# Kernel tuning notes

Measured on AMD Instinct MI355X. Metric: run time of the kernel, lower is better.

Reference implementation:

```python
import jax, jax.numpy as jnp
import numpy as np

B, HP, WP, EMB = 32, 56, 56, 256
HEADS, WX, WY = 8, 7, 7
WS = WX * WY

# relative position index table (constant int lookup, matches torch buffer)
_idx = np.indices((WX, WY)).transpose(1, 2, 0).reshape(WS, 2)
_REL = _idx[None, :, :] - _idx[:, None, :] + np.array([WX - 1, WY - 1])  # [49,49,2]

# shift masks (constants)
_m = WX * (WY // 2)
_row = np.zeros((WS, WS), np.float32)
_row[-_m:, :-_m] = -np.inf
_row[:-_m, -_m:] = -np.inf
# rearrange '(r w1) (c w2) -> (w1 r) (w2 c)' with w1=WX, w2=WY
_col = _row.reshape(WS // WX, WX, WS // WY, WY).transpose(1, 0, 3, 2).reshape(WS, WS)
ROW_MASK = jnp.asarray(_row)
COL_MASK = jnp.asarray(_col)


def setup_inputs() -> dict:
    key = jax.random.key(0)
    k1, k2, k3 = jax.random.split(key, 3)
    x = jax.random.normal(k1, (B, HP, WP, EMB), jnp.float32)
    w1 = jax.random.normal(k2, (EMB, 3 * EMB), jnp.float32) * 0.02
    b1 = jnp.zeros((3 * EMB,), jnp.float32)
    pos_emb = jax.random.normal(k3, (2 * WX - 1, 2 * WY - 1), jnp.float32)
    return {"x": x, "w1": w1, "b1": b1, "pos_emb": pos_emb}


def reference(x, w1, b1, pos_emb):
    Bn, H, W, E = x.shape
    e = E // HEADS
    hdim = float(E) / HEADS
    qkv = x @ w1 + b1                         # [B,H,W,3E]
    qkv = qkv.reshape(Bn, H, W, E, 3)         # (c k): c outer, k inner (interleaved QKV)
    # shifted: roll by (-WX)//2 = -4 for WX=7 (Python floor div, as in source)
    qkv = jnp.roll(qkv, ((-WX) // 2, (-WY) // 2), axis=(1, 2))
    Wh, Ww = H // WX, W // WY
    # split channel (e H): head index is INNER dim, as in source rearrange
    t = qkv.reshape(Bn, Wh, WX, Ww, WY, e, HEADS, 3)
    t = t.transpose(0, 6, 1, 3, 2, 4, 5, 7).reshape(Bn, HEADS, Wh, Ww, WS, e, 3)
    q, k, v = t[..., 0], t[..., 1], t[..., 2]
    attn = jnp.einsum('bhuvqe,bhuvke->bhuvqk', q, k) / jnp.sqrt(
        jnp.asarray(hdim, x.dtype))
    bias = pos_emb[_REL[:, :, 0], _REL[:, :, 1]]   # [49,49]
    attn = attn + bias
    # shift masks on last window row / last window column (corner gets both)
    attn = attn.at[:, :, -1, :, :, :].add(ROW_MASK)
    attn = attn.at[:, :, :, -1, :, :].add(COL_MASK)
    out = jnp.einsum('bhuvqk,bhuvke->bhuvqe', jax.nn.softmax(attn, axis=-1), v)
    # merge back: channel = e*HEADS + h
    out = out.reshape(Bn, HEADS, Wh, Ww, WX, WY, e)
    out = out.transpose(0, 2, 4, 3, 5, 6, 1).reshape(Bn, H, W, E)
    # reverse roll uses WX//2 = +3 (NOT the inverse of -4), faithful to source
    out = jnp.roll(out, (WX // 2, WY // 2), axis=(1, 2))
    return out
```

## Files before the change

### kernel.cpp

```cpp
#include <hip/hip_runtime.h>


typedef short bf16x8 __attribute__((ext_vector_type(8)));
typedef float f32x4 __attribute__((ext_vector_type(4)));
typedef unsigned short u16;
typedef u16 u16x8 __attribute__((ext_vector_type(8)));

#define MFMA16(A, B, C) __builtin_amdgcn_mfma_f32_16x16x32_bf16((A), (B), (C), 0, 0, 0)

__device__ __forceinline__ u16 f2bf(float f) {
  union { float f; unsigned int u; } c; c.f = f;
  unsigned int uu = c.u;
  return (u16)((uu + 0x7fffu + ((uu >> 16) & 1u)) >> 16);
}

#define OFF_A   32768
#define OFF_POS 65536
#define SMEM_BYTES (65536 + 704)

__global__ void prep_w(const float* __restrict__ w1, const float* __restrict__ b1,
                       u16* __restrict__ wT, float* __restrict__ bp) {
  int g = blockIdx.x * 256 + threadIdx.x;
  float val = w1[g];
  int n = g % 768;
  int k = g / 768;
  int t = n % 3, c = n / 3;
  int np = (c & 7) * 96 + t * 32 + (c >> 3);
  wT[np * 256 + k] = f2bf(val);
  if (g < 768) {
    int t2 = g % 3, c2 = g / 3;
    bp[(c2 & 7) * 96 + t2 * 32 + (c2 >> 3)] = b1[g];
  }
}

__launch_bounds__(512, 4)
__global__ void swin_fused(const float* __restrict__ x, const u16* __restrict__ wT,
                           const float* __restrict__ bp, const float* __restrict__ pos,
                           float* __restrict__ out) {
  __shared__ __align__(16) char smem[SMEM_BYTES];
  const int tid  = threadIdx.x;
  const int wave = tid >> 6;
  const int lane = tid & 63;
  const int quad = lane >> 4;
  const int l16  = lane & 15;
  const int blk  = blockIdx.x;
  const int b = blk >> 6, u = (blk >> 3) & 7, v = blk & 7;

  float* sPos = (float*)(smem + OFF_POS);
  if (tid < 169) sPos[tid] = pos[tid];

  {
    const int xbase = b * (56 * 56 * 256);
#pragma unroll
    for (int it = 0; it < 4; ++it) {
      int idx = tid + it * 512;
      int row = idx >> 5;
      int ck  = idx & 31;
      char* dst = smem + OFF_A + row * 512 + ((ck ^ (row & 7)) << 4);
      u16x8 val{};
      if (row < 49) {
        int i = row / 7, j = row % 7;
        int sh = u * 7 + i + 4; if (sh >= 56) sh -= 56;
        int sw = v * 7 + j + 4; if (sw >= 56) sw -= 56;
        const float4* src = (const float4*)(x + xbase + (sh * 56 + sw) * 256 + ck * 8);
        float4 f0 = src[0];
        float4 f1 = src[1];
        val.s0 = f2bf(f0.x); val.s1 = f2bf(f0.y); val.s2 = f2bf(f0.z); val.s3 = f2bf(f0.w);
        val.s4 = f2bf(f1.x); val.s5 = f2bf(f1.y); val.s6 = f2bf(f1.z); val.s7 = f2bf(f1.w);
      }
      *(u16x8*)dst = val;
    }
  }

  float bias[6];
#pragma unroll
  for (int i = 0; i < 6; ++i) bias[i] = bp[wave * 96 + i * 16 + l16];

  __syncthreads();

  const char* sA = smem + OFF_A;
  char* T = smem + wave * 4096;
  bf16x8 qf[4], kf[4], vf[2][2];

#pragma unroll
  for (int t = 0; t < 3; ++t) {
    f32x4 acc[4][2];
#pragma unroll
    for (int m = 0; m < 4; ++m) {
      acc[m][0] = (f32x4){0.f, 0.f, 0.f, 0.f};
      acc[m][1] = (f32x4){0.f, 0.f, 0.f, 0.f};
    }
    const u16* gB0 = wT + (wave * 96 + t * 32 + l16) * 256 + quad * 8;
    const u16* gB1 = gB0 + 16 * 256;
    bf16x8 b0 = *(const bf16x8*)gB0;
    bf16x8 b1 = *(const bf16x8*)gB1;
#pragma unroll
    for (int ks = 0; ks < 8; ++ks) {
      bf16x8 a[4];
#pragma unroll
      for (int m = 0; m < 4; ++m) {
        int row = m * 16 + l16;
        a[m] = *(const bf16x8*)(sA + row * 512 + (((ks * 4 + quad) ^ (row & 7)) << 4));
      }
      bf16x8 b0n, b1n;
      if (ks < 7) {
        b0n = *(const bf16x8*)(gB0 + (ks + 1) * 32);
        b1n = *(const bf16x8*)(gB1 + (ks + 1) * 32);
      }
#pragma unroll
      for (int m = 0; m < 4; ++m) {
        acc[m][0] = MFMA16(a[m], b0, acc[m][0]);
        acc[m][1] = MFMA16(a[m], b1, acc[m][1]);
      }
      if (ks < 7) { b0 = b0n; b1 = b1n; }
    }

    if (t < 2) {
#pragma unroll
      for (int m = 0; m < 4; ++m)
#pragma unroll
        for (int r = 0; r < 4; ++r) {
          int row = m * 16 + quad * 4 + r;
          int sw = (row >> 2) & 3;
          char* base = T + row * 64;
          *(u16*)(base + ((((l16 >> 3) ^ sw) << 4) | ((l16 & 7) << 1)))
              = f2bf(acc[m][0][r] + bias[t * 2]);
          *(u16*)(base + (((((l16 >> 3) + 2) ^ sw) << 4) | ((l16 & 7) << 1)))
              = f2bf(acc[m][1][r] + bias[t * 2 + 1]);
        }
      asm volatile("s_waitcnt lgkmcnt(0)" ::: "memory");
#pragma unroll
      for (int m = 0; m < 4; ++m) {
        int row = m * 16 + l16;
        const bf16x8 fr = *(const bf16x8*)(T + row * 64 + ((quad ^ ((row >> 2) & 3)) << 4));
        if (t == 0) qf[m] = fr; else kf[m] = fr;
      }
      asm volatile("s_waitcnt lgkmcnt(0)" ::: "memory");
    } else {
#pragma unroll
      for (int m = 0; m < 4; ++m)
#pragma unroll
        for (int r = 0; r < 4; ++r) {
          int key = m * 16 + quad * 4 + r;
          int kc = key >> 3, kb = (key & 7) << 1;
#pragma unroll
          for (int i = 0; i < 2; ++i) {
            int ch = i * 16 + l16;
            *(u16*)(T + ch * 128 + (((kc ^ (ch & 7)) << 4) | kb))
                = f2bf(acc[m][i][r] + bias[4 + i]);
          }
        }
      asm volatile("s_waitcnt lgkmcnt(0)" ::: "memory");
    }
  }

#pragma unroll
  for (int ph = 0; ph < 2; ++ph)
#pragma unroll
    for (int n = 0; n < 2; ++n) {
      int ch = n * 16 + l16;
      vf[ph][n] = *(const bf16x8*)(T + ch * 128 + (((ph * 4 + quad) ^ (ch & 7)) << 4));
    }
  asm volatile("s_waitcnt lgkmcnt(0)" ::: "memory");

  int ki[4], kj[4]; bool kok[4], kro[4], kco[4];
#pragma unroll
  for (int n = 0; n < 4; ++n) {
    int k = n * 16 + l16;
    ki[n] = k / 7; kj[n] = k % 7;
    kok[n] = (k < 49);
    kro[n] = (ki[n] >= 4);
    kco[n] = (kj[n] >= 4);
  }
  const bool rowm = (u == 7), colm = (v == 7);
  const float scale = 0.17677669529663687f;

  f32x4 o[4][2];
  {
    char* T2 = T;
#pragma unroll
    for (int m = 0; m < 4; ++m) {
      f32x4 s[4];
#pragma unroll
      for (int n = 0; n < 4; ++n)
        s[n] = MFMA16(qf[m], kf[n], ((f32x4){0.f, 0.f, 0.f, 0.f}));

      float inv[4];
#pragma unroll
      for (int r = 0; r < 4; ++r) {
        int q = m * 16 + quad * 4 + r;
        int qi = q / 7, qj = q % 7;
        bool qro = (qi >= 4), qco = (qj >= 4);
        float vmax = -3e30f;
#pragma unroll
        for (int n = 0; n < 4; ++n) {
          bool bad = (!kok[n]) || (rowm && (qro != kro[n])) || (colm && (qco != kco[n]));
          float sv = bad ? -1e30f
                         : s[n][r] * scale + sPos[(ki[n] - qi + 6) * 13 + (kj[n] - qj + 6)];
          s[n][r] = sv;
          vmax = fmaxf(vmax, sv);
        }
        vmax = fmaxf(vmax, __shfl_xor(vmax, 1));
        vmax = fmaxf(vmax, __shfl_xor(vmax, 2));
        vmax = fmaxf(vmax, __shfl_xor(vmax, 4));
        vmax = fmaxf(vmax, __shfl_xor(vmax, 8));
        float sum = 0.f;
#pragma unroll
        for (int n = 0; n < 4; ++n) {
          float p = __expf(s[n][r] - vmax);
          s[n][r] = p;
          sum += p;
        }
        sum += __shfl_xor(sum, 1);
        sum += __shfl_xor(sum, 2);
        sum += __shfl_xor(sum, 4);
        sum += __shfl_xor(sum, 8);
        inv[r] = 1.f / sum;
      }

#pragma unroll
      for (int n = 0; n < 4; ++n)
#pragma unroll
        for (int r = 0; r < 4; ++r) {
          int row16 = quad * 4 + r;
          int ch = (2 * n + (l16 >> 3) + row16) & 7;
          *(u16*)(T2 + row16 * 128 + ((ch << 4) | ((l16 & 7) << 1))) = f2bf(s[n][r]);
        }
      asm volatile("s_waitcnt lgkmcnt(0)" ::: "memory");
      bf16x8 pa0 = *(const bf16x8*)(T2 + l16 * 128 + ((((quad + l16) & 7)) << 4));
      bf16x8 pa1 = *(const bf16x8*)(T2 + l16 * 128 + (((4 + quad + l16) & 7) << 4));
      asm volatile("s_waitcnt lgkmcnt(0)" ::: "memory");

      o[m][0] = MFMA16(pa0, vf[0][0], ((f32x4){0.f, 0.f, 0.f, 0.f}));
      o[m][0] = MFMA16(pa1, vf[1][0], o[m][0]);
      o[m][1] = MFMA16(pa0, vf[0][1], ((f32x4){0.f, 0.f, 0.f, 0.f}));
      o[m][1] = MFMA16(pa1, vf[1][1], o[m][1]);
#pragma unroll
      for (int i = 0; i < 2; ++i)
#pragma unroll
        for (int r = 0; r < 4; ++r) o[m][i][r] *= inv[r];
    }
  }

  __syncthreads();
  {
    float* oLds = (float*)smem;
    const int hh = wave;
#pragma unroll
    for (int m = 0; m < 4; ++m)
#pragma unroll
      for (int r = 0; r < 4; ++r) {
        int row = m * 16 + quad * 4 + r;
        if (row < 49) {
#pragma unroll
          for (int n = 0; n < 2; ++n) {
            int ci = n * 32 + l16 * 2 + (hh >> 2);
            int cs = ci ^ ((ci >> 3) & 3);
            oLds[row * 260 + cs * 4 + (hh & 3)] = o[m][n][r];
          }
        }
      }
  }
  __syncthreads();

  {
    const int obase = b * (56 * 56 * 256);
    for (int i2 = tid; i2 < 49 * 64; i2 += 512) {
      int row = i2 >> 6, ck = i2 & 63;
      int ii = row / 7, jj = row % 7;
      int dh = u * 7 + ii + 3; if (dh >= 56) dh -= 56;
      int dw = v * 7 + jj + 3; if (dw >= 56) dw -= 56;
      f32x4 val = *(const f32x4*)((const float*)smem + row * 260 + 4 * (ck ^ ((ck >> 3) & 3)));
      *(f32x4*)(out + obase + (dh * 56 + dw) * 256 + ck * 4) = val;
    }
  }
}

extern "C" void kernel_launch(void* const* d_in, const int* in_sizes, int n_in,
                              void* d_out, int out_size, void* d_ws, size_t ws_size,
                              hipStream_t stream) {
  const float* x   = (const float*)d_in[0];
  const float* w1  = (const float*)d_in[1];
  const float* b1  = (const float*)d_in[2];
  const float* pos = (const float*)d_in[3];
  const size_t need = (size_t)768 * 256 * 2 + 768 * 4;
  if (ws_size < need) return;
  u16*   wT = (u16*)d_ws;
  float* bp = (float*)((char*)d_ws + 768 * 256 * 2);
  prep_w<<<768, 256, 0, stream>>>(w1, b1, wT, bp);
  swin_fused<<<2048, 512, 0, stream>>>(x, wT, bp, pos, (float*)d_out);
}
```

Measured before the change: 315.5 us.

## Merge Q/K projection GEMMs, vectorize V stores, and retune LDS swizzles

```diff
diff --git a/kernel.cpp b/kernel.cpp
--- a/kernel.cpp
+++ b/kernel.cpp
@@ -5,6 +5,7 @@
 typedef float f32x4 __attribute__((ext_vector_type(4)));
 typedef unsigned short u16;
 typedef u16 u16x8 __attribute__((ext_vector_type(8)));
+typedef u16 u16x4 __attribute__((ext_vector_type(4)));
 
 #define MFMA16(A, B, C) __builtin_amdgcn_mfma_f32_16x16x32_bf16((A), (B), (C), 0, 0, 0)
 
@@ -16,7 +17,7 @@
 
 #define OFF_A   32768
 #define OFF_POS 65536
-#define SMEM_BYTES (65536 + 704)
+#define SMEM_BYTES (65536 + 896)
 
 __global__ void prep_w(const float* __restrict__ w1, const float* __restrict__ b1,
                        u16* __restrict__ wT, float* __restrict__ bp) {
@@ -47,7 +48,7 @@
   const int b = blk >> 6, u = (blk >> 3) & 7, v = blk & 7;
 
   float* sPos = (float*)(smem + OFF_POS);
-  if (tid < 169) sPos[tid] = pos[tid];
+  if (tid < 169) sPos[(tid / 13) * 16 + tid % 13] = pos[tid];
 
   {
     const int xbase = b * (56 * 56 * 256);
@@ -82,26 +83,70 @@
   char* T = smem + wave * 4096;
   bf16x8 qf[4], kf[4], vf[2][2];
 
-#pragma unroll
-  for (int t = 0; t < 3; ++t) {
+  {
+    f32x4 acc[4][4];
+#pragma unroll
+    for (int m = 0; m < 4; ++m)
+#pragma unroll
+      for (int j = 0; j < 4; ++j) acc[m][j] = (f32x4){0.f, 0.f, 0.f, 0.f};
+    const u16* gB[4];
+#pragma unroll
+    for (int j = 0; j < 4; ++j)
+      gB[j] = wT + (wave * 96 + j * 16 + l16) * 256 + quad * 8;
+#pragma unroll
+    for (int ks = 0; ks < 8; ++ks) {
+      bf16x8 bb[4];
+#pragma unroll
+      for (int j = 0; j < 4; ++j) bb[j] = *(const bf16x8*)(gB[j] + ks * 32);
+#pragma unroll
+      for (int m = 0; m < 4; ++m) {
+        int row = m * 16 + l16;
+        bf16x8 am = *(const bf16x8*)(sA + row * 512 + (((ks * 4 + quad) ^ (row & 7)) << 4));
+#pragma unroll
+        for (int j = 0; j < 4; ++j) acc[m][j] = MFMA16(am, bb[j], acc[m][j]);
+      }
+    }
+
+#pragma unroll
+    for (int t = 0; t < 2; ++t) {
+#pragma unroll
+      for (int m = 0; m < 4; ++m)
+#pragma unroll
+        for (int r = 0; r < 4; ++r) {
+          int row = m * 16 + quad * 4 + r;
+          int sw = (row >> 2) & 3;
+          char* base = T + (row ^ ((row >> 2) & 1)) * 64;
+          *(u16*)(base + ((((l16 >> 3) ^ sw) << 4) | ((l16 & 7) << 1)))
+              = f2bf(acc[m][2 * t + 0][r] + bias[2 * t]);
+          *(u16*)(base + (((((l16 >> 3) + 2) ^ sw) << 4) | ((l16 & 7) << 1)))
+              = f2bf(acc[m][2 * t + 1][r] + bias[2 * t + 1]);
+        }
+      asm volatile("s_waitcnt lgkmcnt(0)" ::: "memory");
+#pragma unroll
+      for (int m = 0; m < 4; ++m) {
+        int row = m * 16 + l16;
+        int sw = (row >> 2) & 3;
+        const bf16x8 fr = *(const bf16x8*)(T + (row ^ ((row >> 2) & 1)) * 64
+                                             + ((quad ^ sw) << 4));
+        if (t == 0) qf[m] = fr; else kf[m] = fr;
+      }
+      asm volatile("s_waitcnt lgkmcnt(0)" ::: "memory");
+    }
+  }
+
+  {
     f32x4 acc[4][2];
 #pragma unroll
     for (int m = 0; m < 4; ++m) {
       acc[m][0] = (f32x4){0.f, 0.f, 0.f, 0.f};
       acc[m][1] = (f32x4){0.f, 0.f, 0.f, 0.f};
     }
-    const u16* gB0 = wT + (wave * 96 + t * 32 + l16) * 256 + quad * 8;
+    const u16* gB0 = wT + (wave * 96 + 64 + l16) * 256 + quad * 8;
     const u16* gB1 = gB0 + 16 * 256;
     bf16x8 b0 = *(const bf16x8*)gB0;
     bf16x8 b1 = *(const bf16x8*)gB1;
 #pragma unroll
     for (int ks = 0; ks < 8; ++ks) {
-      bf16x8 a[4];
-#pragma unroll
-      for (int m = 0; m < 4; ++m) {
-        int row = m * 16 + l16;
-        a[m] = *(const bf16x8*)(sA + row * 512 + (((ks * 4 + quad) ^ (row & 7)) << 4));
-      }
       bf16x8 b0n, b1n;
       if (ks < 7) {
         b0n = *(const bf16x8*)(gB0 + (ks + 1) * 32);
@@ -109,49 +154,30 @@
       }
 #pragma unroll
       for (int m = 0; m < 4; ++m) {
-        acc[m][0] = MFMA16(a[m], b0, acc[m][0]);
-        acc[m][1] = MFMA16(a[m], b1, acc[m][1]);
+        int row = m * 16 + l16;
+        bf16x8 am = *(const bf16x8*)(sA + row * 512 + (((ks * 4 + quad) ^ (row & 7)) << 4));
+        acc[m][0] = MFMA16(am, b0, acc[m][0]);
+        acc[m][1] = MFMA16(am, b1, acc[m][1]);
       }
       if (ks < 7) { b0 = b0n; b1 = b1n; }
     }
 
-    if (t < 2) {
-#pragma unroll
-      for (int m = 0; m < 4; ++m)
-#pragma unroll
-        for (int r = 0; r < 4; ++r) {
-          int row = m * 16 + quad * 4 + r;
-          int sw = (row >> 2) & 3;
-          char* base = T + row * 64;
-          *(u16*)(base + ((((l16 >> 3) ^ sw) << 4) | ((l16 & 7) << 1)))
-              = f2bf(acc[m][0][r] + bias[t * 2]);
-          *(u16*)(base + (((((l16 >> 3) + 2) ^ sw) << 4) | ((l16 & 7) << 1)))
-              = f2bf(acc[m][1][r] + bias[t * 2 + 1]);
-        }
-      asm volatile("s_waitcnt lgkmcnt(0)" ::: "memory");
-#pragma unroll
-      for (int m = 0; m < 4; ++m) {
-        int row = m * 16 + l16;
-        const bf16x8 fr = *(const bf16x8*)(T + row * 64 + ((quad ^ ((row >> 2) & 3)) << 4));
-        if (t == 0) qf[m] = fr; else kf[m] = fr;
-      }
-      asm volatile("s_waitcnt lgkmcnt(0)" ::: "memory");
-    } else {
-#pragma unroll
-      for (int m = 0; m < 4; ++m)
-#pragma unroll
-        for (int r = 0; r < 4; ++r) {
-          int key = m * 16 + quad * 4 + r;
-          int kc = key >> 3, kb = (key & 7) << 1;
-#pragma unroll
-          for (int i = 0; i < 2; ++i) {
-            int ch = i * 16 + l16;
-            *(u16*)(T + ch * 128 + (((kc ^ (ch & 7)) << 4) | kb))
-                = f2bf(acc[m][i][r] + bias[4 + i]);
-          }
-        }
-      asm volatile("s_waitcnt lgkmcnt(0)" ::: "memory");
-    }
+#pragma unroll
+    for (int m = 0; m < 4; ++m) {
+      int kc = m * 2 + (quad >> 1);
+      int hb = (quad & 1) << 3;
+#pragma unroll
+      for (int i = 0; i < 2; ++i) {
+        u16x4 w;
+        w.x = f2bf(acc[m][i][0] + bias[4 + i]);
+        w.y = f2bf(acc[m][i][1] + bias[4 + i]);
+        w.z = f2bf(acc[m][i][2] + bias[4 + i]);
+        w.w = f2bf(acc[m][i][3] + bias[4 + i]);
+        int ch = i * 16 + l16;
+        *(u16x4*)(T + ch * 128 + (((kc ^ (ch & 7)) << 4) | hb)) = w;
+      }
+    }
+    asm volatile("s_waitcnt lgkmcnt(0)" ::: "memory");
   }
 
 #pragma unroll
@@ -191,12 +217,13 @@
         int q = m * 16 + quad * 4 + r;
         int qi = q / 7, qj = q % 7;
         bool qro = (qi >= 4), qco = (qj >= 4);
+        int cm = 102 - qi * 16 - qj;
         float vmax = -3e30f;
 #pragma unroll
         for (int n = 0; n < 4; ++n) {
           bool bad = (!kok[n]) || (rowm && (qro != kro[n])) || (colm && (qco != kco[n]));
           float sv = bad ? -1e30f
-                         : s[n][r] * scale + sPos[(ki[n] - qi + 6) * 13 + (kj[n] - qj + 6)];
+                         : s[n][r] * scale + sPos[ki[n] * 16 + kj[n] + cm];
           s[n][r] = sv;
           vmax = fmaxf(vmax, sv);
         }
@@ -223,12 +250,12 @@
 #pragma unroll
         for (int r = 0; r < 4; ++r) {
           int row16 = quad * 4 + r;
-          int ch = (2 * n + (l16 >> 3) + row16) & 7;
+          int ch = (2 * n + (l16 >> 3) + 2 * quad) & 7;
           *(u16*)(T2 + row16 * 128 + ((ch << 4) | ((l16 & 7) << 1))) = f2bf(s[n][r]);
         }
       asm volatile("s_waitcnt lgkmcnt(0)" ::: "memory");
-      bf16x8 pa0 = *(const bf16x8*)(T2 + l16 * 128 + ((((quad + l16) & 7)) << 4));
-      bf16x8 pa1 = *(const bf16x8*)(T2 + l16 * 128 + (((4 + quad + l16) & 7) << 4));
+      bf16x8 pa0 = *(const bf16x8*)(T2 + l16 * 128 + (((quad + 2 * (l16 >> 2)) & 7) << 4));
+      bf16x8 pa1 = *(const bf16x8*)(T2 + l16 * 128 + (((4 + quad + 2 * (l16 >> 2)) & 7) << 4));
       asm volatile("s_waitcnt lgkmcnt(0)" ::: "memory");
 
       o[m][0] = MFMA16(pa0, vf[0][0], ((f32x4){0.f, 0.f, 0.f, 0.f}));
@@ -252,10 +279,12 @@
       for (int r = 0; r < 4; ++r) {
         int row = m * 16 + quad * 4 + r;
         if (row < 49) {
+          int t4 = row >> 2;
+          int fr = (t4 + (t4 >> 1)) & 7;
 #pragma unroll
           for (int n = 0; n < 2; ++n) {
             int ci = n * 32 + l16 * 2 + (hh >> 2);
-            int cs = ci ^ ((ci >> 3) & 3);
+            int cs = ci ^ fr;
             oLds[row * 260 + cs * 4 + (hh & 3)] = o[m][n][r];
           }
         }
@@ -270,7 +299,9 @@
       int ii = row / 7, jj = row % 7;
       int dh = u * 7 + ii + 3; if (dh >= 56) dh -= 56;
       int dw = v * 7 + jj + 3; if (dw >= 56) dw -= 56;
-      f32x4 val = *(const f32x4*)((const float*)smem + row * 260 + 4 * (ck ^ ((ck >> 3) & 3)));
+      int t4 = row >> 2;
+      int fr = (t4 + (t4 >> 1)) & 7;
+      f32x4 val = *(const f32x4*)((const float*)smem + row * 260 + 4 * (ck ^ fr));
       *(f32x4*)(out + obase + (dh * 56 + dw) * 256 + ck * 4) = val;
     }
   }
```

Result: slower. 326.1 us (+3.3%).
